# Kernel tuning notes

Hardware: AMD Instinct MI355X
Metric: run time of the kernel (lower is better)

Reference implementation:

```python
import jax, jax.numpy as jnp
import numpy as np
from math import sqrt

B, L, S, H, E, D = 4, 1024, 1024, 16, 64, 64


def setup_inputs() -> dict:
    key = jax.random.key(0)
    k0, k1, k2, k3 = jax.random.split(key, 4)
    queries = jax.random.normal(k0, (B, L, H, E), dtype=jnp.float32)
    keys = jax.random.normal(k1, (B, S, H, E), dtype=jnp.float32)
    values = jax.random.normal(k2, (B, S, H, D), dtype=jnp.float32)
    # RealFormer residual logits from a "previous layer", shape [B,H,L,S]
    prev_logits = jax.random.normal(k3, (B, H, L, S), dtype=jnp.float32) * 0.1
    # Triangular causal mask: True above the diagonal (positions to mask out)
    attn_mask = jnp.triu(jnp.ones((L, S), dtype=bool), k=1)[None, None]  # [1,1,L,S] broadcasts over B
    attn_mask = jnp.broadcast_to(attn_mask, (B, 1, L, S))
    return {"queries": queries, "keys": keys, "values": values,
            "prev_logits": prev_logits, "attn_mask": attn_mask}


def reference(queries, keys, values, prev_logits, attn_mask):
    # queries [B,L,H,E], keys [B,S,H,E], values [B,S,H,D]
    scale = 1.0 / sqrt(queries.shape[-1])
    scores = jnp.einsum('blhe,bshe->bhls', queries, keys) * scale  # [B,H,L,S]
    # RealFormer residual
    scores = scores + prev_logits
    # causal masking with dtype-min (matches torch.finfo(dtype).min masked_fill)
    neg_inf = jnp.finfo(scores.dtype).min
    scores = jnp.where(attn_mask, neg_inf, scores)
    A = jax.nn.softmax(scores, axis=-1)  # dropout p=0.0 -> identity (eval/reference mode)
    # Faithful to source: einsum 'bhls,bshd->bhls' sums only over d,
    # i.e. V[b,h,l,s] = A[b,h,l,s] * sum_d values[b,s,h,d]
    V = jnp.einsum('bhls,bshd->bhls', A, values)  # [B,H,L,S]
    # return_logits=True, output_attention=False -> (V, None, scores); drop the None
    return V, scores
```

## Files before the change

kernel.cpp:

```cpp
#include <hip/hip_runtime.h>
#include <cfloat>

#define B_ 4
#define L_ 1024
#define S_ 1024
#define H_ 16
#define E_ 64
#define TL 32
#define TS 128
#define NT (S_ / TS)

#define MASK_VAL (-3.3895313892515355e38f)

typedef __attribute__((ext_vector_type(8))) short short8;
typedef __attribute__((ext_vector_type(4))) float f32x4;

__device__ __forceinline__ unsigned short f32_to_bf16(float x) {
    unsigned int u = __float_as_uint(x);
    u += 0x7FFFu + ((u >> 16) & 1u);
    return (unsigned short)(u >> 16);
}

__device__ __forceinline__ short8 pack8v(const f32x4 a, const f32x4 b, float s) {
    short8 r;
    r[0] = (short)f32_to_bf16(a[0] * s); r[1] = (short)f32_to_bf16(a[1] * s);
    r[2] = (short)f32_to_bf16(a[2] * s); r[3] = (short)f32_to_bf16(a[3] * s);
    r[4] = (short)f32_to_bf16(b[0] * s); r[5] = (short)f32_to_bf16(b[1] * s);
    r[6] = (short)f32_to_bf16(b[2] * s); r[7] = (short)f32_to_bf16(b[3] * s);
    return r;
}

__device__ __forceinline__ void nt_store4(float* p, float a, float b, float c, float d) {
    f32x4 v = {a, b, c, d};
    __builtin_nontemporal_store(v, (f32x4*)p);
}
__device__ __forceinline__ f32x4 nt_load4(const float* p) {
    return __builtin_nontemporal_load((const f32x4*)p);
}

__global__ __launch_bounds__(256) void vsum_kernel(const float* __restrict__ values,
                                                   float* __restrict__ vsum_t) {
    int t = threadIdx.x;
    int rg = blockIdx.x * 16 + (t >> 4);
    int c = t & 15;
    float4 v = ((const float4*)(values + (long)rg * 64))[c];
    float p = v.x + v.y + v.z + v.w;
    p += __shfl_xor(p, 1);
    p += __shfl_xor(p, 2);
    p += __shfl_xor(p, 4);
    p += __shfl_xor(p, 8);
    if (c == 0) {
        int b = rg >> 14;
        int s = (rg >> 4) & (S_ - 1);
        int h = rg & (H_ - 1);
        vsum_t[(((b << 4) + h) << 10) + s] = p;
    }
}

template <int USE_WS>
__global__ __launch_bounds__(512) void attn_kernel(
    const float* __restrict__ Qg,
    const float* __restrict__ Kg,
    const float* __restrict__ prev,
    const float* __restrict__ vsum,
    const float* __restrict__ values,
    float* __restrict__ outV,
    float* __restrict__ outS)
{
    __shared__ __align__(16) short Ksh[TS * E_];
    __shared__ __align__(16) float Dsh[TL * TS];
    __shared__ __align__(16) float Vsl[S_];

    const int tid  = threadIdx.x;
    const int lane = tid & 63;
    const int wave = tid >> 6;
    const int bid  = blockIdx.x;
    const int jj   = bid >> 3;
    const int bh   = ((bid & 7) << 3) | (jj & 7);
    const int lt   = 31 - (jj >> 3);
    const int b    = bh >> 4;
    const int h    = bh & 15;
    const int row0 = lt << 5;

    if (USE_WS) {
        if (tid < 256) {
            float4 v = ((const float4*)(vsum + ((long)bh << 10)))[tid];
            *((float4*)&Vsl[tid << 2]) = v;
        }
    } else {
#pragma unroll
        for (int i = 0; i < 2; ++i) {
            int s = tid + (i << 9);
            const float4* vp = (const float4*)(values + (((long)((b << 10) + s) << 10) + (h << 6)));
            float a = 0.f;
#pragma unroll
            for (int j = 0; j < 16; ++j) { float4 t4 = vp[j]; a += t4.x + t4.y + t4.z + t4.w; }
            Vsl[s] = a;
        }
    }

    const int mcol  = lane & 15;
    const int mg    = lane >> 4;
    const int strip = wave & 1;
    const int qrow  = row0 + (strip << 4) + mcol;
    short8 qf0, qf1;
    {
        const float* qp = Qg + (((long)((b << 10) + qrow) << 10) + (h << 6));
        f32x4 a0 = *(const f32x4*)(qp + (mg << 3));
        f32x4 a1 = *(const f32x4*)(qp + (mg << 3) + 4);
        f32x4 a2 = *(const f32x4*)(qp + 32 + (mg << 3));
        f32x4 a3 = *(const f32x4*)(qp + 32 + (mg << 3) + 4);
        qf0 = pack8v(a0, a1, 1.0f);
        qf1 = pack8v(a2, a3, 1.0f);
    }

    const int cg   = lane & 31;
    const int half = lane >> 5;
    const int r0   = (wave << 2) + (half << 1);
    const int r1   = r0 + 1;
    const int rg0  = row0 + r0;
    const int rg1  = row0 + r1;
    const int maxrow = row0 + TL - 1;
    const long outbase = (long)bh << 20;

    const int sr  = tid >> 2;
    const int qtr = tid & 3;
    f32x4 kv0, kv1, kv2, kv3;
#define KLOAD(STC) do { \
        const f32x4* kp = (const f32x4*)(Kg + (((long)((b << 10) + ((STC) * TS + sr)) << 10) + (h << 6) + (qtr << 4))); \
        kv0 = kp[0]; kv1 = kp[1]; kv2 = kp[2]; kv3 = kp[3]; \
    } while (0)

    KLOAD(0);

    float sc0[NT][4], sc1[NT][4];
    float sum0 = 0.f, sum1 = 0.f;

#pragma unroll
    for (int st = 0; st < NT; ++st) {
        const int s0 = st * TS;
        const int colb = s0 + (cg << 2);
        if (s0 > maxrow) {
            nt_store4(outS + outbase + (long)rg0 * S_ + colb, MASK_VAL, MASK_VAL, MASK_VAL, MASK_VAL);
            nt_store4(outS + outbase + (long)rg1 * S_ + colb, MASK_VAL, MASK_VAL, MASK_VAL, MASK_VAL);
            nt_store4(outV + outbase + (long)rg0 * S_ + colb, 0.f, 0.f, 0.f, 0.f);
            nt_store4(outV + outbase + (long)rg1 * S_ + colb, 0.f, 0.f, 0.f, 0.f);
        } else {
            f32x4 p0 = nt_load4(prev + outbase + (long)rg0 * S_ + colb);
            f32x4 p1 = nt_load4(prev + outbase + (long)rg1 * S_ + colb);

            {
                int base = sr << 6;
                int xr = sr & 7;
                *(short8*)&Ksh[base + ((((qtr << 1) + 0) ^ xr) << 3)] = pack8v(kv0, kv1, 0.125f);
                *(short8*)&Ksh[base + ((((qtr << 1) + 1) ^ xr) << 3)] = pack8v(kv2, kv3, 0.125f);
            }
            if (s0 + TS <= maxrow) { KLOAD(st + 1); }
            __syncthreads();

#pragma unroll
            for (int i = 0; i < 2; ++i) {
                const int ss  = ((wave >> 1) << 1) + i;
                const int lsr = (ss << 4) + mcol;
                const int xr  = mcol & 7;
                short8 a0 = *(const short8*)&Ksh[(lsr << 6) + (((0 + mg) ^ xr) << 3)];
                short8 a1 = *(const short8*)&Ksh[(lsr << 6) + (((4 + mg) ^ xr) << 3)];
                f32x4 acc = {0.f, 0.f, 0.f, 0.f};
                acc = __builtin_amdgcn_mfma_f32_16x16x32_bf16(a0, qf0, acc, 0, 0, 0);
                acc = __builtin_amdgcn_mfma_f32_16x16x32_bf16(a1, qf1, acc, 0, 0, 0);
                const int lrow = (strip << 4) + mcol;
                const int qd   = (ss << 2) + mg;
                *(f32x4*)&Dsh[(lrow << 7) + ((qd ^ (lrow & 7)) << 2)] = acc;
            }
            __syncthreads();

            f32x4 d0 = *(const f32x4*)&Dsh[(r0 << 7) + ((cg ^ (r0 & 7)) << 2)];
            f32x4 d1 = *(const f32x4*)&Dsh[(r1 << 7) + ((cg ^ (r1 & 7)) << 2)];
#pragma unroll
            for (int j = 0; j < 4; ++j) {
                float t0 = d0[j] + p0[j];
                float t1 = d1[j] + p1[j];
                sc0[st][j] = (colb + j > rg0) ? MASK_VAL : t0;
                sc1[st][j] = (colb + j > rg1) ? MASK_VAL : t1;
                sum0 += __expf(sc0[st][j]);
                sum1 += __expf(sc1[st][j]);
            }
        }
    }

#pragma unroll
    for (int m = 1; m <= 16; m <<= 1) {
        sum0 += __shfl_xor(sum0, m);
        sum1 += __shfl_xor(sum1, m);
    }
    const float inv0 = 1.0f / sum0;
    const float inv1 = 1.0f / sum1;

#pragma unroll
    for (int st = 0; st < NT; ++st) {
        const int s0 = st * TS;
        if (s0 > maxrow) continue;
        const int colb = s0 + (cg << 2);
        f32x4 vv = *(const f32x4*)&Vsl[colb];
        nt_store4(outS + outbase + (long)rg0 * S_ + colb,
                  sc0[st][0], sc0[st][1], sc0[st][2], sc0[st][3]);
        nt_store4(outS + outbase + (long)rg1 * S_ + colb,
                  sc1[st][0], sc1[st][1], sc1[st][2], sc1[st][3]);
        nt_store4(outV + outbase + (long)rg0 * S_ + colb,
                  __expf(sc0[st][0]) * inv0 * vv[0],
                  __expf(sc0[st][1]) * inv0 * vv[1],
                  __expf(sc0[st][2]) * inv0 * vv[2],
                  __expf(sc0[st][3]) * inv0 * vv[3]);
        nt_store4(outV + outbase + (long)rg1 * S_ + colb,
                  __expf(sc1[st][0]) * inv1 * vv[0],
                  __expf(sc1[st][1]) * inv1 * vv[1],
                  __expf(sc1[st][2]) * inv1 * vv[2],
                  __expf(sc1[st][3]) * inv1 * vv[3]);
    }
#undef KLOAD
}

extern "C" void kernel_launch(void* const* d_in, const int* in_sizes, int n_in,
                              void* d_out, int out_size, void* d_ws, size_t ws_size,
                              hipStream_t stream) {
    const float* Qg   = (const float*)d_in[0];
    const float* Kg   = (const float*)d_in[1];
    const float* Vg   = (const float*)d_in[2];
    const float* prev = (const float*)d_in[3];

    float* outV = (float*)d_out;
    float* outS = outV + (long)B_ * H_ * L_ * S_;

    const size_t vsum_bytes = (size_t)B_ * H_ * S_ * sizeof(float);
    const int grid = B_ * H_ * (L_ / TL);
    if (ws_size >= vsum_bytes) {
        float* vsum_t = (float*)d_ws;
        vsum_kernel<<<(B_ * S_ * H_) / 16, 256, 0, stream>>>(Vg, vsum_t);
        attn_kernel<1><<<grid, 512, 0, stream>>>(Qg, Kg, prev, vsum_t, Vg, outV, outS);
    } else {
        attn_kernel<0><<<grid, 512, 0, stream>>>(Qg, Kg, prev, nullptr, Vg, outV, outS);
    }
}
```

Baseline: 153.1 us.

## Double-buffer K and score tiles, software-pipeline epilogue, prefetch prev logits

Double-buffers the K and score shared-memory tiles so the MFMA for tile st overlaps the softmax epilogue of tile st-1, which drops one barrier per tile. It also issues the prev-logit loads one tile ahead, writes scores out during the first pass, and keeps exp values so the second pass does not recompute them. Fully masked tiles are written up front. The cost is doubled LDS use, which may cut occupancy, plus more registers holding the prefetched prev values and exp arrays.

```diff
diff --git a/kernel.cpp b/kernel.cpp
--- a/kernel.cpp
+++ b/kernel.cpp
@@ -67,8 +67,8 @@
     float* __restrict__ outV,
     float* __restrict__ outS)
 {
-    __shared__ __align__(16) short Ksh[TS * E_];
-    __shared__ __align__(16) float Dsh[TL * TS];
+    __shared__ __align__(16) short Ksh[2][TS * E_];
+    __shared__ __align__(16) float Dsh[2][TL * TS];
     __shared__ __align__(16) float Vsl[S_];
 
     const int tid  = threadIdx.x;
@@ -121,7 +121,16 @@
     const int rg0  = row0 + r0;
     const int rg1  = row0 + r1;
     const int maxrow = row0 + TL - 1;
+    const int NC   = (maxrow >> 7) + 1;
     const long outbase = (long)bh << 20;
+
+    for (int st = NC; st < NT; ++st) {
+        const int colb = st * TS + (cg << 2);
+        nt_store4(outS + outbase + (long)rg0 * S_ + colb, MASK_VAL, MASK_VAL, MASK_VAL, MASK_VAL);
+        nt_store4(outS + outbase + (long)rg1 * S_ + colb, MASK_VAL, MASK_VAL, MASK_VAL, MASK_VAL);
+        nt_store4(outV + outbase + (long)rg0 * S_ + colb, 0.f, 0.f, 0.f, 0.f);
+        nt_store4(outV + outbase + (long)rg1 * S_ + colb, 0.f, 0.f, 0.f, 0.f);
+    }
 
     const int sr  = tid >> 2;
     const int qtr = tid & 3;
@@ -131,62 +140,76 @@
         kv0 = kp[0]; kv1 = kp[1]; kv2 = kp[2]; kv3 = kp[3]; \
     } while (0)
 
+    float ev0[NT][4], ev1[NT][4];
+    f32x4 pv0[NT], pv1[NT];
+    float sum0 = 0.f, sum1 = 0.f;
+
     KLOAD(0);
-
-    float sc0[NT][4], sc1[NT][4];
-    float sum0 = 0.f, sum1 = 0.f;
-
-#pragma unroll
-    for (int st = 0; st < NT; ++st) {
-        const int s0 = st * TS;
-        const int colb = s0 + (cg << 2);
-        if (s0 > maxrow) {
-            nt_store4(outS + outbase + (long)rg0 * S_ + colb, MASK_VAL, MASK_VAL, MASK_VAL, MASK_VAL);
-            nt_store4(outS + outbase + (long)rg1 * S_ + colb, MASK_VAL, MASK_VAL, MASK_VAL, MASK_VAL);
-            nt_store4(outV + outbase + (long)rg0 * S_ + colb, 0.f, 0.f, 0.f, 0.f);
-            nt_store4(outV + outbase + (long)rg1 * S_ + colb, 0.f, 0.f, 0.f, 0.f);
-        } else {
-            f32x4 p0 = nt_load4(prev + outbase + (long)rg0 * S_ + colb);
-            f32x4 p1 = nt_load4(prev + outbase + (long)rg1 * S_ + colb);
-
+    pv0[0] = nt_load4(prev + outbase + (long)rg0 * S_ + (cg << 2));
+    pv1[0] = nt_load4(prev + outbase + (long)rg1 * S_ + (cg << 2));
+
+#define EPI(c) do { \
+        const float* DB = &Dsh[(c) & 1][0]; \
+        f32x4 d0 = *(const f32x4*)&DB[(r0 << 7) + ((cg ^ (r0 & 7)) << 2)]; \
+        f32x4 d1 = *(const f32x4*)&DB[(r1 << 7) + ((cg ^ (r1 & 7)) << 2)]; \
+        const int colb = (c) * TS + (cg << 2); \
+        float sA[4], sB[4]; \
+        _Pragma("unroll") \
+        for (int j = 0; j < 4; ++j) { \
+            float t0 = d0[j] + pv0[c][j]; \
+            float t1 = d1[j] + pv1[c][j]; \
+            sA[j] = (colb + j > rg0) ? MASK_VAL : t0; \
+            sB[j] = (colb + j > rg1) ? MASK_VAL : t1; \
+            float e0 = __expf(sA[j]); ev0[c][j] = e0; sum0 += e0; \
+            float e1 = __expf(sB[j]); ev1[c][j] = e1; sum1 += e1; \
+        } \
+        nt_store4(outS + outbase + (long)rg0 * S_ + colb, sA[0], sA[1], sA[2], sA[3]); \
+        nt_store4(outS + outbase + (long)rg1 * S_ + colb, sB[0], sB[1], sB[2], sB[3]); \
+    } while (0)
+
+#pragma unroll
+    for (int st = 0; st <= NT; ++st) {
+        if (st < NC) {
             {
+                short* KB = &Ksh[st & 1][0];
                 int base = sr << 6;
                 int xr = sr & 7;
-                *(short8*)&Ksh[base + ((((qtr << 1) + 0) ^ xr) << 3)] = pack8v(kv0, kv1, 0.125f);
-                *(short8*)&Ksh[base + ((((qtr << 1) + 1) ^ xr) << 3)] = pack8v(kv2, kv3, 0.125f);
+                *(short8*)&KB[base + ((((qtr << 1) + 0) ^ xr) << 3)] = pack8v(kv0, kv1, 0.125f);
+                *(short8*)&KB[base + ((((qtr << 1) + 1) ^ xr) << 3)] = pack8v(kv2, kv3, 0.125f);
             }
-            if (s0 + TS <= maxrow) { KLOAD(st + 1); }
-            __syncthreads();
-
-#pragma unroll
-            for (int i = 0; i < 2; ++i) {
-                const int ss  = ((wave >> 1) << 1) + i;
-                const int lsr = (ss << 4) + mcol;
-                const int xr  = mcol & 7;
-                short8 a0 = *(const short8*)&Ksh[(lsr << 6) + (((0 + mg) ^ xr) << 3)];
-                short8 a1 = *(const short8*)&Ksh[(lsr << 6) + (((4 + mg) ^ xr) << 3)];
-                f32x4 acc = {0.f, 0.f, 0.f, 0.f};
-                acc = __builtin_amdgcn_mfma_f32_16x16x32_bf16(a0, qf0, acc, 0, 0, 0);
-                acc = __builtin_amdgcn_mfma_f32_16x16x32_bf16(a1, qf1, acc, 0, 0, 0);
-                const int lrow = (strip << 4) + mcol;
-                const int qd   = (ss << 2) + mg;
-                *(f32x4*)&Dsh[(lrow << 7) + ((qd ^ (lrow & 7)) << 2)] = acc;
+            if (st + 1 < NC) {
+                KLOAD(st + 1);
+                pv0[st + 1] = nt_load4(prev + outbase + (long)rg0 * S_ + (st + 1) * TS + (cg << 2));
+                pv1[st + 1] = nt_load4(prev + outbase + (long)rg1 * S_ + (st + 1) * TS + (cg << 2));
             }
             __syncthreads();
-
-            f32x4 d0 = *(const f32x4*)&Dsh[(r0 << 7) + ((cg ^ (r0 & 7)) << 2)];
-            f32x4 d1 = *(const f32x4*)&Dsh[(r1 << 7) + ((cg ^ (r1 & 7)) << 2)];
-#pragma unroll
-            for (int j = 0; j < 4; ++j) {
-                float t0 = d0[j] + p0[j];
-                float t1 = d1[j] + p1[j];
-                sc0[st][j] = (colb + j > rg0) ? MASK_VAL : t0;
-                sc1[st][j] = (colb + j > rg1) ? MASK_VAL : t1;
-                sum0 += __expf(sc0[st][j]);
-                sum1 += __expf(sc1[st][j]);
+            {
+                const short* KB = &Ksh[st & 1][0];
+                float* DB = &Dsh[st & 1][0];
+#pragma unroll
+                for (int i = 0; i < 2; ++i) {
+                    const int ss  = ((wave >> 1) << 1) + i;
+                    const int lsr = (ss << 4) + mcol;
+                    const int xr  = mcol & 7;
+                    short8 a0 = *(const short8*)&KB[(lsr << 6) + (((0 + mg) ^ xr) << 3)];
+                    short8 a1 = *(const short8*)&KB[(lsr << 6) + (((4 + mg) ^ xr) << 3)];
+                    f32x4 acc = {0.f, 0.f, 0.f, 0.f};
+                    acc = __builtin_amdgcn_mfma_f32_16x16x32_bf16(a0, qf0, acc, 0, 0, 0);
+                    acc = __builtin_amdgcn_mfma_f32_16x16x32_bf16(a1, qf1, acc, 0, 0, 0);
+                    const int lrow = (strip << 4) + mcol;
+                    const int qd   = (ss << 2) + mg;
+                    *(f32x4*)&DB[(lrow << 7) + ((qd ^ (lrow & 7)) << 2)] = acc;
+                }
             }
-        }
-    }
+        } else if (st == NC) {
+            __syncthreads();
+        }
+        if (st >= 1 && st - 1 < NC) {
+            EPI(st - 1);
+        }
+    }
+#undef EPI
+#undef KLOAD
 
 #pragma unroll
     for (int m = 1; m <= 16; m <<= 1) {
@@ -198,26 +221,17 @@
 
 #pragma unroll
     for (int st = 0; st < NT; ++st) {
-        const int s0 = st * TS;
-        if (s0 > maxrow) continue;
-        const int colb = s0 + (cg << 2);
-        f32x4 vv = *(const f32x4*)&Vsl[colb];
-        nt_store4(outS + outbase + (long)rg0 * S_ + colb,
-                  sc0[st][0], sc0[st][1], sc0[st][2], sc0[st][3]);
-        nt_store4(outS + outbase + (long)rg1 * S_ + colb,
-                  sc1[st][0], sc1[st][1], sc1[st][2], sc1[st][3]);
-        nt_store4(outV + outbase + (long)rg0 * S_ + colb,
-                  __expf(sc0[st][0]) * inv0 * vv[0],
-                  __expf(sc0[st][1]) * inv0 * vv[1],
-                  __expf(sc0[st][2]) * inv0 * vv[2],
-                  __expf(sc0[st][3]) * inv0 * vv[3]);
-        nt_store4(outV + outbase + (long)rg1 * S_ + colb,
-                  __expf(sc1[st][0]) * inv1 * vv[0],
-                  __expf(sc1[st][1]) * inv1 * vv[1],
-                  __expf(sc1[st][2]) * inv1 * vv[2],
-                  __expf(sc1[st][3]) * inv1 * vv[3]);
-    }
-#undef KLOAD
+        if (st < NC) {
+            const int colb = st * TS + (cg << 2);
+            f32x4 vv = *(const f32x4*)&Vsl[colb];
+            nt_store4(outV + outbase + (long)rg0 * S_ + colb,
+                      ev0[st][0] * inv0 * vv[0], ev0[st][1] * inv0 * vv[1],
+                      ev0[st][2] * inv0 * vv[2], ev0[st][3] * inv0 * vv[3]);
+            nt_store4(outV + outbase + (long)rg1 * S_ + colb,
+                      ev1[st][0] * inv1 * vv[0], ev1[st][1] * inv1 * vv[1],
+                      ev1[st][2] * inv1 * vv[2], ev1[st][3] * inv1 * vv[3]);
+        }
+    }
 }
 
 extern "C" void kernel_launch(void* const* d_in, const int* in_sizes, int n_in,
```

Measured after the change: 172.2 us. 12.5% more time.
